# Kernel tuning notes

Measured on AMD Instinct MI355X. Metric: run time of the kernel, lower is better.

The kernel has to match this reference:

```python
import jax, jax.numpy as jnp
import numpy as np

B, T, D, H, E = 32, 512, 768, 12, 6  # batch, seq(=input_size), n_embd, num_heads, per-head dim
DFF = 4 * D
EPS = 1e-5


def setup_inputs() -> dict:
    key = jax.random.key(0)
    ks = jax.random.split(key, 10)
    s = 0.02
    return {
        "x": jax.random.normal(ks[0], (B, T, D), jnp.float32),
        "Wq": jax.random.normal(ks[1], (H, D, E), jnp.float32) * s,
        "Wk": jax.random.normal(ks[2], (H, D, E), jnp.float32) * s,
        "Wv": jax.random.normal(ks[3], (H, D, E), jnp.float32) * s,
        "Wo": jax.random.normal(ks[4], (H * E, D), jnp.float32) * s,
        "bo": jnp.zeros((D,), jnp.float32),
        "W1": jax.random.normal(ks[5], (D, DFF), jnp.float32) * s,
        "b1": jnp.zeros((DFF,), jnp.float32),
        "W2": jax.random.normal(ks[6], (DFF, D), jnp.float32) * s,
        "b2": jnp.zeros((D,), jnp.float32),
        "g1": jnp.ones((D,), jnp.float32),
        "beta1": jnp.zeros((D,), jnp.float32),
        "g2": jnp.ones((D,), jnp.float32),
        "beta2": jnp.zeros((D,), jnp.float32),
    }


def _layernorm(x, g, b):
    m = jnp.mean(x, axis=-1, keepdims=True)
    v = jnp.var(x, axis=-1, keepdims=True)  # biased, matches torch LayerNorm
    return (x - m) * jax.lax.rsqrt(v + EPS) * g + b


def reference(x, Wq, Wk, Wv, Wo, bo, W1, b1, W2, b2, g1, beta1, g2, beta2):
    # --- pre-LN multi-head causal attention (dropout = identity, eval mode) ---
    xn = _layernorm(x, g1, beta1)
    q = jnp.einsum("btd,hde->bhte", xn, Wq)
    k = jnp.einsum("btd,hde->bhte", xn, Wk)
    v = jnp.einsum("btd,hde->bhte", xn, Wv)
    scores = jnp.einsum("bhte,bhse->bhts", q, k) * (E ** -0.5)
    causal = jnp.tril(jnp.ones((T, T), dtype=bool))
    scores = jnp.where(causal, scores, -jnp.inf)
    w = jax.nn.softmax(scores, axis=-1)
    o = jnp.einsum("bhts,bhse->bhte", w, v)
    o = o.transpose(0, 2, 1, 3).reshape(B, T, H * E)  # concat heads -> [B,T,72]
    x = x + o @ Wo + bo
    # --- pre-LN feed-forward ---
    y = _layernorm(x, g2, beta2)
    ff = jax.nn.relu(y @ W1 + b1) @ W2 + b2
    return x + ff
```

## Files before the change

kernel.cpp:

```cpp
#include <hip/hip_runtime.h>
#include <hip/hip_bf16.h>

#define BT 16384
#define DIM 768
#define NH 12
#define DFF 3072

typedef __attribute__((ext_vector_type(8))) short short8;
typedef __attribute__((ext_vector_type(4))) float floatx4;
typedef __attribute__((ext_vector_type(4))) unsigned short ushort4b;

using bf16 = __hip_bfloat16;

static __device__ __forceinline__ float b2f(bf16 v) { return __bfloat162float(v); }
static __device__ __forceinline__ bf16 f2b(float v) { return __float2bfloat16(v); }

static __device__ __forceinline__ void gload_lds16(const void* g, void* l) {
    __builtin_amdgcn_global_load_lds(
        (const __attribute__((address_space(1))) unsigned int*)g,
        (__attribute__((address_space(3))) unsigned int*)l, 16, 0, 0);
}

__global__ __launch_bounds__(256) void pack_small_kernel(
    const float* __restrict__ Wq, const float* __restrict__ Wk, const float* __restrict__ Wv,
    const float* __restrict__ Wo, bf16* __restrict__ wqkv, bf16* __restrict__ wo_t)
{
    int i = blockIdx.x * 256 + threadIdx.x;
    const int S0 = 256 * 768, S1 = 768 * 96;
    if (i < S0) {
        int c = i / 768, dd = i % 768;
        float v = 0.f;
        if (c < 216) {
            int sel = c / 72, cc = c % 72, h = cc / 6, e = cc % 6;
            const float* W = (sel == 0) ? Wq : (sel == 1) ? Wk : Wv;
            v = W[((size_t)h * 768 + dd) * 6 + e];
        }
        wqkv[i] = f2b(v);
    } else if ((i -= S0) < S1) {
        int n = i / 96, r = i % 96;
        wo_t[i] = f2b(r < 72 ? Wo[r * 768 + n] : 0.f);
    }
}

__global__ __launch_bounds__(256) void transpose_kernel(
    const float* __restrict__ in, bf16* __restrict__ out, int R, int C)
{
    __shared__ float t[32][33];
    int c0 = blockIdx.x * 32, r0 = blockIdx.y * 32;
    int cx = threadIdx.x & 31, ry = threadIdx.x >> 5;
#pragma unroll
    for (int j = 0; j < 4; j++)
        t[ry + j * 8][cx] = in[(size_t)(r0 + ry + j * 8) * C + c0 + cx];
    __syncthreads();
    int rx = cx, cy = ry;
#pragma unroll
    for (int j = 0; j < 4; j++)
        out[(size_t)(c0 + cy + j * 8) * R + r0 + rx] = f2b(t[rx][cy + j * 8]);
}

__global__ __launch_bounds__(192) void ln_kernel(
    const float* __restrict__ x, const float* __restrict__ g, const float* __restrict__ be,
    bf16* __restrict__ out)
{
    int row = blockIdx.x;
    int tid = threadIdx.x;
    const float4* xr = (const float4*)(x + (size_t)row * DIM);
    float4 v = xr[tid];
    float s = v.x + v.y + v.z + v.w;
    float s2 = v.x * v.x + v.y * v.y + v.z * v.z + v.w * v.w;
#pragma unroll
    for (int off = 32; off; off >>= 1) {
        s += __shfl_down(s, off);
        s2 += __shfl_down(s2, off);
    }
    __shared__ float red[6];
    int wv = tid >> 6, ln = tid & 63;
    if (ln == 0) { red[wv] = s; red[3 + wv] = s2; }
    __syncthreads();
    float ts = red[0] + red[1] + red[2];
    float ts2 = red[3] + red[4] + red[5];
    float mean = ts * (1.f / 768.f);
    float var = ts2 * (1.f / 768.f) - mean * mean;
    float rstd = rsqrtf(var + 1e-5f);
    int c = tid * 4;
    float o0 = (v.x - mean) * rstd * g[c + 0] + be[c + 0];
    float o1 = (v.y - mean) * rstd * g[c + 1] + be[c + 1];
    float o2 = (v.z - mean) * rstd * g[c + 2] + be[c + 2];
    float o3 = (v.w - mean) * rstd * g[c + 3] + be[c + 3];
    bf16 h0 = f2b(o0), h1 = f2b(o1), h2 = f2b(o2), h3 = f2b(o3);
    ushort4b pk;
    pk[0] = *(unsigned short*)&h0; pk[1] = *(unsigned short*)&h1;
    pk[2] = *(unsigned short*)&h2; pk[3] = *(unsigned short*)&h3;
    *(ushort4b*)(out + (size_t)row * DIM + c) = pk;
}

template <int NSLAB, bool RELU, bool BIAS, bool RES, bool BF16OUT>
__global__ __launch_bounds__(256) void gemm_kernel(
    const bf16* __restrict__ A, const bf16* __restrict__ Bt,
    const float* __restrict__ bias, const float* __restrict__ res,
    void* __restrict__ Cv, int M, int N, int K)
{
    constexpr int SMEM_BYTES = BF16OUT ? (128 * 136 * 2) : (NSLAB * 2 * 128 * 32 * 2);
    __shared__ __align__(16) char smem[SMEM_BYTES];
    bf16* lA = (bf16*)smem;
    bf16* lB = lA + NSLAB * 128 * 32;

    const int tid = threadIdx.x;
    const int bm = blockIdx.x * 128;
    const int bn = blockIdx.y * 128;
    const int wave = tid >> 6, lane = tid & 63;
    const int wm = (wave >> 1) * 64, wn = (wave & 1) * 64;
    const int quad = lane >> 4, l16 = lane & 15;
    const int lrow = lane >> 2;
    const int lkc = (lane & 3) * 8;

    floatx4 acc[4][4] = {};

    for (int k0 = 0; k0 < K; k0 += NSLAB * 32) {
#pragma unroll
        for (int s = 0; s < NSLAB; s++) {
#pragma unroll
            for (int it = 0; it < 2; it++) {
                int r = wave * 32 + it * 16;
                gload_lds16(A + (size_t)(bm + r + lrow) * K + k0 + s * 32 + lkc,
                            lA + s * 4096 + r * 32);
                gload_lds16(Bt + (size_t)(bn + r + lrow) * K + k0 + s * 32 + lkc,
                            lB + s * 4096 + r * 32);
            }
        }
        __syncthreads();
#pragma unroll
        for (int s = 0; s < NSLAB; s++) {
            short8 af[4], bfr[4];
#pragma unroll
            for (int mt = 0; mt < 4; mt++)
                af[mt] = *(const short8*)(lA + s * 4096 + (wm + mt * 16 + l16) * 32 + quad * 8);
#pragma unroll
            for (int nt = 0; nt < 4; nt++)
                bfr[nt] = *(const short8*)(lB + s * 4096 + (wn + nt * 16 + l16) * 32 + quad * 8);
#pragma unroll
            for (int mt = 0; mt < 4; mt++)
#pragma unroll
                for (int nt = 0; nt < 4; nt++)
                    acc[mt][nt] = __builtin_amdgcn_mfma_f32_16x16x32_bf16(af[mt], bfr[nt], acc[mt][nt], 0, 0, 0);
        }
        __syncthreads();
    }

    if constexpr (BF16OUT) {
        bf16* ltile = (bf16*)smem;
#pragma unroll
        for (int mt = 0; mt < 4; mt++) {
#pragma unroll
            for (int nt = 0; nt < 4; nt++) {
                int tc = wn + nt * 16 + l16;
#pragma unroll
                for (int r = 0; r < 4; r++) {
                    int tr = wm + mt * 16 + quad * 4 + r;
                    float v0 = acc[mt][nt][r];
                    if constexpr (BIAS) v0 += bias[bn + tc];
                    if constexpr (RELU) v0 = fmaxf(v0, 0.f);
                    ltile[tr * 136 + tc] = f2b(v0);
                }
            }
        }
        __syncthreads();
        bf16* C = (bf16*)Cv;
        int rr0 = tid >> 4, col8 = (tid & 15) * 8;
        int gc = bn + col8;
#pragma unroll
        for (int p = 0; p < 8; p++) {
            int rr = p * 16 + rr0;
            if (gc < N)
                *(short8*)(C + (size_t)(bm + rr) * N + gc) =
                    *(const short8*)(ltile + rr * 136 + col8);
        }
    } else {
        float* C = (float*)Cv;
#pragma unroll
        for (int mt = 0; mt < 4; mt++) {
#pragma unroll
            for (int nt = 0; nt < 4; nt++) {
                int gc = bn + wn + nt * 16 + l16;
                if (gc < N) {
#pragma unroll
                    for (int r = 0; r < 4; r++) {
                        int gr = bm + wm + mt * 16 + quad * 4 + r;
                        float v0 = acc[mt][nt][r];
                        if constexpr (BIAS) v0 += bias[gc];
                        if constexpr (RES) v0 += res[(size_t)gr * N + gc];
                        if constexpr (RELU) v0 = fmaxf(v0, 0.f);
                        C[(size_t)gr * N + gc] = v0;
                    }
                }
            }
        }
    }
}

__global__ __launch_bounds__(256) void attn_kernel(const bf16* __restrict__ qkv, bf16* __restrict__ o_pad)
{
    int blk = blockIdx.x;
    int half = blk & 1;
    int bh = blk >> 1;
    int b = bh / NH, h = bh % NH;
    int wave = threadIdx.x >> 6, lane = threadIdx.x & 63;
    const int jmap0[4] = {0, 2, 5, 7}, jmap1[4] = {1, 3, 4, 6};
    int j = half ? jmap1[wave] : jmap0[wave];
    int t = j * 64 + lane;
    int smax = half ? 448 : 512;

    __shared__ float ks[512 * 6];
    __shared__ float vs[512 * 6];
    const bf16* base = qkv + (size_t)b * 512 * 216;
    for (int i = threadIdx.x; i < smax * 6; i += 256) {
        int s = i / 6, e = i % 6;
        ks[i] = b2f(base[s * 216 + 72 + h * 6 + e]);
        vs[i] = b2f(base[s * 216 + 144 + h * 6 + e]);
    }
    __syncthreads();

    float q0 = b2f(base[t * 216 + h * 6 + 0]);
    float q1 = b2f(base[t * 216 + h * 6 + 1]);
    float q2 = b2f(base[t * 216 + h * 6 + 2]);
    float q3 = b2f(base[t * 216 + h * 6 + 3]);
    float q4 = b2f(base[t * 216 + h * 6 + 4]);
    float q5 = b2f(base[t * 216 + h * 6 + 5]);

    const float scale = 0.4082482904638630f;
    float m = -1e30f, l = 0.f;
    float o0 = 0, o1 = 0, o2 = 0, o3 = 0, o4 = 0, o5 = 0;
    for (int s = 0; s <= t; s++) {
        const float* kk = &ks[s * 6];
        float sc = (q0 * kk[0] + q1 * kk[1] + q2 * kk[2] + q3 * kk[3] + q4 * kk[4] + q5 * kk[5]) * scale;
        float nm = fmaxf(m, sc);
        float alpha = __expf(m - nm);
        float p = __expf(sc - nm);
        l = l * alpha + p;
        const float* vv = &vs[s * 6];
        o0 = o0 * alpha + p * vv[0];
        o1 = o1 * alpha + p * vv[1];
        o2 = o2 * alpha + p * vv[2];
        o3 = o3 * alpha + p * vv[3];
        o4 = o4 * alpha + p * vv[4];
        o5 = o5 * alpha + p * vv[5];
        m = nm;
    }
    float inv = 1.f / l;
    bf16* orow = o_pad + (size_t)(b * 512 + t) * 96 + h * 6;
    orow[0] = f2b(o0 * inv);
    orow[1] = f2b(o1 * inv);
    orow[2] = f2b(o2 * inv);
    orow[3] = f2b(o3 * inv);
    orow[4] = f2b(o4 * inv);
    orow[5] = f2b(o5 * inv);
}

extern "C" void kernel_launch(void* const* d_in, const int* in_sizes, int n_in,
                              void* d_out, int out_size, void* d_ws, size_t ws_size,
                              hipStream_t stream)
{
    const float* x   = (const float*)d_in[0];
    const float* Wq  = (const float*)d_in[1];
    const float* Wk  = (const float*)d_in[2];
    const float* Wv  = (const float*)d_in[3];
    const float* Wo  = (const float*)d_in[4];
    const float* bo  = (const float*)d_in[5];
    const float* W1  = (const float*)d_in[6];
    const float* b1  = (const float*)d_in[7];
    const float* W2  = (const float*)d_in[8];
    const float* b2  = (const float*)d_in[9];
    const float* g1  = (const float*)d_in[10];
    const float* be1 = (const float*)d_in[11];
    const float* g2  = (const float*)d_in[12];
    const float* be2 = (const float*)d_in[13];

    char* ws = (char*)d_ws;
    size_t off = 0;
    auto alloc = [&](size_t bytes) {
        void* p = ws + off;
        off = (off + bytes + 255) & ~(size_t)255;
        return p;
    };
    bf16*  xn    = (bf16*)alloc((size_t)BT * DIM * 2);
    bf16*  qkvb  = (bf16*)alloc((size_t)BT * 216 * 2);
    bf16*  o_pad = (bf16*)alloc((size_t)BT * 96 * 2);
    float* x1    = (float*)alloc((size_t)BT * DIM * 4);
    bf16*  ffb   = (bf16*)alloc((size_t)BT * DFF * 2);
    bf16*  wqkv  = (bf16*)alloc((size_t)256 * 768 * 2);
    bf16*  wo_t  = (bf16*)alloc((size_t)768 * 96 * 2);
    bf16*  w1t   = (bf16*)alloc((size_t)3072 * 768 * 2);
    bf16*  w2t   = (bf16*)alloc((size_t)768 * 3072 * 2);

    const int PACK_N = 256 * 768 + 768 * 96;
    pack_small_kernel<<<(PACK_N + 255) / 256, 256, 0, stream>>>(Wq, Wk, Wv, Wo, wqkv, wo_t);
    transpose_kernel<<<dim3(3072 / 32, 768 / 32), 256, 0, stream>>>(W1, w1t, 768, 3072);
    transpose_kernel<<<dim3(768 / 32, 3072 / 32), 256, 0, stream>>>(W2, w2t, 3072, 768);

    ln_kernel<<<BT, 192, 0, stream>>>(x, g1, be1, xn);
    gemm_kernel<2, false, false, false, true><<<dim3(128, 2), 256, 0, stream>>>(
        xn, wqkv, nullptr, nullptr, qkvb, BT, 216, 768);
    attn_kernel<<<32 * NH * 2, 256, 0, stream>>>(qkvb, o_pad);
    gemm_kernel<1, false, true, true, false><<<dim3(128, 6), 256, 0, stream>>>(
        o_pad, wo_t, bo, x, x1, BT, 768, 96);
    ln_kernel<<<BT, 192, 0, stream>>>(x1, g2, be2, xn);
    gemm_kernel<2, true, true, false, true><<<dim3(128, 24), 256, 0, stream>>>(
        xn, w1t, b1, nullptr, ffb, BT, 3072, 768);
    gemm_kernel<2, false, true, true, false><<<dim3(128, 6), 256, 0, stream>>>(
        ffb, w2t, b2, x1, (float*)d_out, BT, 768, 3072);
}
```

Before: 465.5 us.

## Add 256x256-tile pipelined MFMA GEMM for FFN up and down projections

```diff
diff --git a/kernel.cpp b/kernel.cpp
--- a/kernel.cpp
+++ b/kernel.cpp
@@ -198,6 +198,139 @@
     }
 }
 
+template <bool RELU, bool BIAS, bool RES, bool BF16OUT>
+__global__ __launch_bounds__(512, 2) void gemm256_kernel(
+    const bf16* __restrict__ A, const bf16* __restrict__ Bt,
+    const float* __restrict__ bias, const float* __restrict__ res,
+    void* __restrict__ Cv, int M, int N, int K)
+{
+    extern __shared__ __align__(16) char smem[];
+    const int NT = K >> 6;
+    const int nbm = M >> 8;
+    const int nwg = nbm * (N >> 8);
+    int idx = blockIdx.x;
+    idx = (idx & 7) * (nwg >> 3) + (idx >> 3);
+    const int bm = (idx % nbm) << 8;
+    const int bn = (idx / nbm) << 8;
+
+    const int tid = threadIdx.x;
+    const int w = tid >> 6, lane = tid & 63;
+    const int wm = w >> 2, wn = w & 3;
+    const int l16 = lane & 15, quad = lane >> 4;
+
+    const int rstg = (w >> 1) * 16 + (lane >> 2);
+    const int cstg = (w & 1) * 32 + ((((lane & 3) * 8)) ^ ((lane & 32) ? 16 : 0));
+    const bf16* aSrc = A + (size_t)(bm + rstg) * K + cstg;
+    const bf16* bSrc = Bt + (size_t)(bn + rstg) * K + cstg;
+    char* dstBase = smem + w * 1024;
+
+    const int xr = (quad * 16) ^ ((l16 & 8) ? 32 : 0);
+    const int aOff = wm * 16384 + l16 * 64 + xr;
+    const int bOff = 32768 + wn * 8192 + l16 * 64 + xr;
+
+#define STAGE(P, ISB, H, T) { \
+    const bf16* _s = ((ISB) ? bSrc : aSrc) + ((size_t)((H) * 128) * K + (size_t)(T) * 64); \
+    char* _d = dstBase + (P) * 65536 + (ISB) * 32768 + (H) * 16384; \
+    gload_lds16(_s, _d); \
+    gload_lds16(_s + (size_t)64 * K, _d + 8192); }
+
+#define BARX() asm volatile("s_barrier" ::: "memory")
+#define VMW(N_) asm volatile("s_waitcnt vmcnt(" #N_ ")" ::: "memory")
+
+    floatx4 acc[8][4] = {};
+    short8 a[4][2], b[2][2][2];
+
+#define LDA(QM, CB) { _Pragma("unroll") for (int fm = 0; fm < 4; fm++) { \
+    _Pragma("unroll") for (int s = 0; s < 2; s++) \
+        a[fm][s] = *(const short8*)((CB) + aOff + (QM) * 8192 + fm * 2048 + s * 1024); } }
+#define LDB(QN, CB) { _Pragma("unroll") for (int fn = 0; fn < 2; fn++) { \
+    _Pragma("unroll") for (int s = 0; s < 2; s++) \
+        b[QN][fn][s] = *(const short8*)((CB) + bOff + (QN) * 4096 + fn * 2048 + s * 1024); } }
+#define MM(QM, QN) { __builtin_amdgcn_s_setprio(1); \
+    _Pragma("unroll") for (int fm = 0; fm < 4; fm++) { \
+    _Pragma("unroll") for (int fn = 0; fn < 2; fn++) { \
+    _Pragma("unroll") for (int s = 0; s < 2; s++) \
+        acc[(QM)*4+fm][(QN)*2+fn] = __builtin_amdgcn_mfma_f32_16x16x32_bf16( \
+            a[fm][s], b[QN][fn][s], acc[(QM)*4+fm][(QN)*2+fn], 0, 0, 0); } } \
+    __builtin_amdgcn_s_setprio(0); }
+
+    STAGE(0, 1, 0, 0); STAGE(0, 1, 1, 0); STAGE(0, 0, 0, 0); STAGE(0, 0, 1, 0);
+    STAGE(1, 1, 0, 1); STAGE(1, 1, 1, 1); STAGE(1, 0, 0, 1);
+    VMW(6);
+    BARX();
+
+    for (int g = 0; g < NT; ++g) {
+        const int p = g & 1, pn = p ^ 1;
+        const char* cb = smem + p * 65536;
+        LDA(0, cb); LDB(0, cb);
+        if (g + 1 < NT) STAGE(pn, 0, 1, g + 1);
+        BARX(); MM(0, 0); BARX();
+        LDB(1, cb);
+        if (g + 2 < NT) STAGE(p, 1, 0, g + 2);
+        BARX(); MM(0, 1); BARX();
+        LDA(1, cb);
+        if (g + 2 < NT) STAGE(p, 1, 1, g + 2);
+        BARX(); MM(1, 0); BARX();
+        if (g + 2 < NT) STAGE(p, 0, 0, g + 2);
+        BARX(); MM(1, 1);
+        if (g < NT - 2) { VMW(6); } else { VMW(0); }
+        BARX();
+    }
+
+    if constexpr (BF16OUT) {
+        bf16* lt = (bf16*)smem;
+#pragma unroll
+        for (int RF = 0; RF < 8; RF++) {
+            const int row = wm * 128 + (RF >> 2) * 64 + (RF & 3) * 16 + quad * 4;
+#pragma unroll
+            for (int CF = 0; CF < 4; CF++) {
+                const int col = wn * 64 + (CF >> 1) * 32 + (CF & 1) * 16 + l16;
+                float bv = BIAS ? bias[bn + col] : 0.f;
+#pragma unroll
+                for (int rr = 0; rr < 4; rr++) {
+                    float v = acc[RF][CF][rr] + bv;
+                    if constexpr (RELU) v = fmaxf(v, 0.f);
+                    lt[(row + rr) * 280 + col] = f2b(v);
+                }
+            }
+        }
+        asm volatile("s_waitcnt lgkmcnt(0)" ::: "memory");
+        BARX();
+        bf16* C = (bf16*)Cv;
+#pragma unroll
+        for (int it = 0; it < 16; it++) {
+            int c = it * 512 + tid;
+            int rr = c >> 5, c8 = (c & 31) * 8;
+            *(short8*)(C + (size_t)(bm + rr) * N + bn + c8) =
+                *(const short8*)(lt + rr * 280 + c8);
+        }
+    } else {
+        float* C = (float*)Cv;
+#pragma unroll
+        for (int RF = 0; RF < 8; RF++) {
+            const int gr = bm + wm * 128 + (RF >> 2) * 64 + (RF & 3) * 16 + quad * 4;
+#pragma unroll
+            for (int CF = 0; CF < 4; CF++) {
+                const int gc = bn + wn * 64 + (CF >> 1) * 32 + (CF & 1) * 16 + l16;
+                float bv = BIAS ? bias[gc] : 0.f;
+#pragma unroll
+                for (int rr = 0; rr < 4; rr++) {
+                    float v = acc[RF][CF][rr] + bv;
+                    if constexpr (RES) v += res[(size_t)(gr + rr) * N + gc];
+                    if constexpr (RELU) v = fmaxf(v, 0.f);
+                    C[(size_t)(gr + rr) * N + gc] = v;
+                }
+            }
+        }
+    }
+#undef STAGE
+#undef BARX
+#undef VMW
+#undef LDA
+#undef LDB
+#undef MM
+}
+
 __global__ __launch_bounds__(256) void attn_kernel(const bf16* __restrict__ qkv, bf16* __restrict__ o_pad)
 {
     int blk = blockIdx.x;
@@ -292,6 +425,11 @@
     bf16*  w1t   = (bf16*)alloc((size_t)3072 * 768 * 2);
     bf16*  w2t   = (bf16*)alloc((size_t)768 * 3072 * 2);
 
+    hipFuncSetAttribute(reinterpret_cast<const void*>(&gemm256_kernel<true, true, false, true>),
+                        hipFuncAttributeMaxDynamicSharedMemorySize, 256 * 280 * 2);
+    hipFuncSetAttribute(reinterpret_cast<const void*>(&gemm256_kernel<false, true, true, false>),
+                        hipFuncAttributeMaxDynamicSharedMemorySize, 131072);
+
     const int PACK_N = 256 * 768 + 768 * 96;
     pack_small_kernel<<<(PACK_N + 255) / 256, 256, 0, stream>>>(Wq, Wk, Wv, Wo, wqkv, wo_t);
     transpose_kernel<<<dim3(3072 / 32, 768 / 32), 256, 0, stream>>>(W1, w1t, 768, 3072);
@@ -304,8 +442,8 @@
     gemm_kernel<1, false, true, true, false><<<dim3(128, 6), 256, 0, stream>>>(
         o_pad, wo_t, bo, x, x1, BT, 768, 96);
     ln_kernel<<<BT, 192, 0, stream>>>(x1, g2, be2, xn);
-    gemm_kernel<2, true, true, false, true><<<dim3(128, 24), 256, 0, stream>>>(
+    gemm256_kernel<true, true, false, true><<<768, 512, 256 * 280 * 2, stream>>>(
         xn, w1t, b1, nullptr, ffb, BT, 3072, 768);
-    gemm_kernel<2, false, true, true, false><<<dim3(128, 6), 256, 0, stream>>>(
+    gemm256_kernel<false, true, true, false><<<192, 512, 131072, stream>>>(
         ffb, w2t, b2, x1, (float*)d_out, BT, 768, 3072);
 }
```

After: 444.7 us. 4.5% less time.
